# Kernel optimization log

Hardware: AMD Instinct MI355X
Metric: run time of the kernel (lower is better)

The kernel has to match this reference:

```python
import jax, jax.numpy as jnp
import numpy as np

N_EMBD = 1024
N_HEAD = 16
B, T, T_MEM = 4, 1024, 1024


def setup_inputs() -> dict:
    key = jax.random.key(0)
    ks = jax.random.split(key, 11)
    s = 1.0 / np.sqrt(N_EMBD)
    inp = {
        "q_in": jax.random.normal(ks[0], (B, T, N_EMBD), jnp.float32),
        "k_in": jax.random.normal(ks[1], (B, T_MEM, N_EMBD), jnp.float32),
        "v_in": jax.random.normal(ks[2], (B, T_MEM, N_EMBD), jnp.float32),
        "Wq": jax.random.normal(ks[3], (N_EMBD, N_EMBD), jnp.float32) * s,
        "bq": jnp.zeros((N_EMBD,), jnp.float32),
        "Wk": jax.random.normal(ks[4], (N_EMBD, N_EMBD), jnp.float32) * s,
        "bk": jnp.zeros((N_EMBD,), jnp.float32),
        "Wv": jax.random.normal(ks[5], (N_EMBD, N_EMBD), jnp.float32) * s,
        "bv": jnp.zeros((N_EMBD,), jnp.float32),
        "Wo": jax.random.normal(ks[6], (N_EMBD, N_EMBD), jnp.float32) * s,
        "bo": jnp.zeros((N_EMBD,), jnp.float32),
    }
    return inp


def reference(q_in, k_in, v_in, Wq, bq, Wk, bk, Wv, bv, Wo, bo):
    b, t, c = q_in.shape
    t_mem = k_in.shape[1]
    h = N_HEAD
    hs = c // h
    # torch Linear: x @ W.T + b
    q = (q_in @ Wq.T + bq).reshape(b, t, h, hs).transpose(0, 2, 1, 3)      # [b,h,t,hs]
    k = (k_in @ Wk.T + bk).reshape(b, t_mem, h, hs).transpose(0, 2, 1, 3)  # [b,h,tm,hs]
    v = (v_in @ Wv.T + bv).reshape(b, t_mem, h, hs).transpose(0, 2, 1, 3)
    att = jnp.einsum('bhtd,bhsd->bhts', q, k) * (1.0 / np.sqrt(hs))        # [b,h,t,tm]
    att = jax.nn.softmax(att, axis=-1)
    # dropout is identity (pdrop=0 / eval mode)
    y = jnp.einsum('bhts,bhsd->bhtd', att, v)                              # [b,h,t,hs]
    y = y.transpose(0, 2, 1, 3).reshape(b, t, c)
    y = y @ Wo.T + bo
    attention = att.mean(axis=1)                                           # [b,t,tm]
    return (y, attention)
```

## Files before the change

### kernel.cpp

```cpp
#include <hip/hip_runtime.h>

typedef unsigned short ushort_t;
typedef __attribute__((ext_vector_type(8))) __bf16 bf16x8;
typedef __attribute__((ext_vector_type(4))) float f32x4;

#define GLD(src, lds) __builtin_amdgcn_global_load_lds( \
    (const __attribute__((address_space(1))) void*)(src), \
    (__attribute__((address_space(3))) void*)(lds), 16, 0, 0)

#if __has_builtin(__builtin_amdgcn_exp2f)
#define EXP2(x) __builtin_amdgcn_exp2f(x)
#else
#define EXP2(x) __expf((x) * 0.69314718f)
#endif
#define QK_SCALE 0.18033688f

static __device__ __forceinline__ f32x4 mfma16(bf16x8 a, bf16x8 b, f32x4 c){
  return __builtin_amdgcn_mfma_f32_16x16x32_bf16(a, b, c, 0, 0, 0);
}
static __device__ __forceinline__ ushort_t f2bf(float f){
  unsigned u = __float_as_uint(f);
  return (ushort_t)((u + 0x7FFFu + ((u >> 16) & 1u)) >> 16);
}

template<int ROWS>
static __device__ __forceinline__ void stage64(const ushort_t* __restrict__ g, size_t rstride,
                                               ushort_t* lds, int tid){
#pragma unroll
  for (int r = 0; r < ROWS/32; ++r){
    int li = r*256 + tid;
    int row = li >> 3, ch = li & 7;
    GLD(g + (size_t)row*rstride + ((ch ^ (row & 7)) << 3),
        (char*)lds + (r*256 + (tid >> 6)*64)*16);
  }
}
static __device__ __forceinline__ bf16x8 frag64(const ushort_t* lds, int row, int ch){
  return *(const bf16x8*)((const char*)lds + row*128 + ((ch ^ (row & 7)) << 4));
}

static __device__ __forceinline__ void stage32(const ushort_t* __restrict__ g, size_t rstride,
                                               ushort_t* lds, int tid){
#pragma unroll
  for (int r = 0; r < 2; ++r){
    int li = r*256 + tid;
    int row = li >> 2, ch = li & 3;
    GLD(g + (size_t)row*rstride + ((ch ^ ((row >> 1) & 3)) << 3),
        (char*)lds + (r*256 + (tid >> 6)*64)*16);
  }
}
static __device__ __forceinline__ bf16x8 frag32(const ushort_t* lds, int row, int ch){
  return *(const bf16x8*)((const char*)lds + row*64 + ((ch ^ ((row >> 1) & 3)) << 4));
}

__global__ __launch_bounds__(256) void cast_all(const float* __restrict__ q,
    const float* __restrict__ k, const float* __restrict__ v,
    const float* __restrict__ wq, const float* __restrict__ wk,
    const float* __restrict__ wv, const float* __restrict__ wo,
    char* __restrict__ ws)
{
  const size_t MB = 1024*1024;
  int i = blockIdx.x*256 + threadIdx.x;
  const float* src; ushort_t* dst; int j;
  if (i < 1048576){ src = q; dst = (ushort_t*)(ws); j = i; }
  else if (i < 2097152){ src = k; dst = (ushort_t*)(ws + 8*MB); j = i - 1048576; }
  else if (i < 3145728){ src = v; dst = (ushort_t*)(ws + 16*MB); j = i - 2097152; }
  else {
    int t = i - 3145728, w = t >> 18; j = t & 262143;
    src = w==0 ? wq : w==1 ? wk : w==2 ? wv : wo;
    dst = (ushort_t*)(ws + (24 + 2*(size_t)w)*MB);
  }
  float4 x = ((const float4*)src)[j];
  ushort4 o;
  o.x = f2bf(x.x); o.y = f2bf(x.y); o.z = f2bf(x.z); o.w = f2bf(x.w);
  ((ushort4*)dst)[j] = o;
}

template<int MODE>
static __device__ __forceinline__ void gemm_body(const ushort_t* __restrict__ A,
    const ushort_t* __restrict__ B, const float* __restrict__ bias,
    void* __restrict__ Cout, int bx, char* smem)
{
  constexpr int K = 1024;
  ushort_t* As0 = (ushort_t*)smem;
  ushort_t* As1 = (ushort_t*)(smem + 8192);
  ushort_t* Bs0 = (ushort_t*)(smem + 16384);
  ushort_t* Bs1 = (ushort_t*)(smem + 24576);
  const int tid = threadIdx.x, lane = tid & 63, wv = tid >> 6;
  const int fr = lane & 15, fq = lane >> 4;
  const int wr = wv >> 1, wc = wv & 1;
  const int brow0 = ((bx & 7) * 4 + ((bx >> 3) & 3)) * 128;
  const int bcol0 = (bx >> 5) * 128;

  const f32x4 zero = {0.f, 0.f, 0.f, 0.f};
  f32x4 acc[4][4];
#pragma unroll
  for (int m = 0; m < 4; ++m)
#pragma unroll
    for (int n = 0; n < 4; ++n) acc[m][n] = zero;

  stage32(A + (size_t)brow0*K, K, As0, tid);
  stage32(B + (size_t)bcol0*K, K, Bs0, tid);
  __syncthreads();

  for (int kt = 0; kt < K/32; ++kt){
    const int cur = kt & 1;
    ushort_t* Ac = cur ? As1 : As0;
    ushort_t* Bc = cur ? Bs1 : Bs0;
    ushort_t* An = cur ? As0 : As1;
    ushort_t* Bn = cur ? Bs0 : Bs1;
    if (kt < K/32 - 1){
      stage32(A + (size_t)brow0*K + (kt+1)*32, K, An, tid);
      stage32(B + (size_t)bcol0*K + (kt+1)*32, K, Bn, tid);
    }
    bf16x8 af[4], bfg[4];
#pragma unroll
    for (int m = 0; m < 4; ++m) af[m]  = frag32(Ac, wr*64 + m*16 + fr, fq);
#pragma unroll
    for (int n = 0; n < 4; ++n) bfg[n] = frag32(Bc, wc*64 + n*16 + fr, fq);
    __builtin_amdgcn_s_setprio(1);
#pragma unroll
    for (int m = 0; m < 4; ++m)
#pragma unroll
      for (int n = 0; n < 4; ++n)
        acc[m][n] = mfma16(af[m], bfg[n], acc[m][n]);
    __builtin_amdgcn_s_setprio(0);
    __syncthreads();
  }

#pragma unroll
  for (int n = 0; n < 4; ++n){
    const int colg = bcol0 + wc*64 + n*16 + fr;
    const float bv = bias[colg];
#pragma unroll
    for (int m = 0; m < 4; ++m){
      const int rowg0 = brow0 + wr*64 + m*16 + fq*4;
      if (MODE == 1){
        int b = rowg0 >> 10, t = rowg0 & 1023, h = colg >> 6, d = colg & 63;
        ushort4 o;
        o.x = f2bf(acc[m][n][0] + bv); o.y = f2bf(acc[m][n][1] + bv);
        o.z = f2bf(acc[m][n][2] + bv); o.w = f2bf(acc[m][n][3] + bv);
        *(ushort4*)((ushort_t*)Cout + (((size_t)(b*16 + h))*64 + d)*1024 + t) = o;
      } else {
#pragma unroll
        for (int r = 0; r < 4; ++r){
          const int rowg = rowg0 + r;
          float val = acc[m][n][r] + bv;
          if (MODE == 0){
            int b = rowg >> 10, t = rowg & 1023, h = colg >> 6, d = colg & 63;
            ((ushort_t*)Cout)[(((size_t)(b*16 + h))*1024 + t)*64 + d] = f2bf(val);
          } else {
            ((float*)Cout)[(size_t)rowg*1024 + colg] = val;
          }
        }
      }
    }
  }
}

__global__ __launch_bounds__(256) void gemm_qkv(const ushort_t* qb, const ushort_t* kb,
    const ushort_t* vb, const ushort_t* wqb, const ushort_t* wkb, const ushort_t* wvb,
    const float* bq, const float* bk, const float* bv,
    ushort_t* Qm, ushort_t* Km, ushort_t* Vtm)
{
  __shared__ char smem[32768];
  int id = blockIdx.x >> 8, bx = blockIdx.x & 255;
  if (id == 0)      gemm_body<0>(qb, wqb, bq, Qm,  bx, smem);
  else if (id == 1) gemm_body<0>(kb, wkb, bk, Km,  bx, smem);
  else              gemm_body<1>(vb, wvb, bv, Vtm, bx, smem);
}

static __device__ __forceinline__ void attmean_body(const ushort_t* __restrict__ Q,
    const ushort_t* __restrict__ Kmat, const float* __restrict__ Lrow,
    float* __restrict__ attOut, int nb, char* smem)
{
  ushort_t* Qs0 = (ushort_t*)smem;
  ushort_t* Qs1 = (ushort_t*)(smem + 8192);
  ushort_t* Ks0 = (ushort_t*)(smem + 16384);
  ushort_t* Ks1 = (ushort_t*)(smem + 32768);
  const int tid = threadIdx.x, lane = tid & 63, wv = tid >> 6;
  const int fr = lane & 15, fq = lane >> 4;
  const int c_ = nb & 7, k_ = nb >> 3;
  const int b = c_ >> 1;
  const int rem = (c_ & 1)*64 + k_;
  const int t0 = (rem >> 3) * 64, s0 = (rem & 7) * 128;

  const f32x4 zero = {0.f, 0.f, 0.f, 0.f};
  f32x4 acc[2][4];
#pragma unroll
  for (int c = 0; c < 2; ++c)
#pragma unroll
    for (int n = 0; n < 4; ++n) acc[c][n] = zero;

  stage64<64>(Q + ((size_t)(b*16)*1024 + t0)*64, 64, Qs0, tid);
  stage64<128>(Kmat + ((size_t)(b*16)*1024 + s0)*64, 64, Ks0, tid);
  __syncthreads();

  for (int h = 0; h < 16; ++h){
    const int cur = h & 1;
    ushort_t* Qc = cur ? Qs1 : Qs0;
    ushort_t* Kc = cur ? Ks1 : Ks0;
    ushort_t* Qn = cur ? Qs0 : Qs1;
    ushort_t* Kn = cur ? Ks0 : Ks1;
    if (h < 15){
      stage64<64>(Q + ((size_t)(b*16 + h+1)*1024 + t0)*64, 64, Qn, tid);
      stage64<128>(Kmat + ((size_t)(b*16 + h+1)*1024 + s0)*64, 64, Kn, tid);
    }
    const int bh = b*16 + h;
    bf16x8 qf0 = frag64(Qc, wv*16 + fr, fq);
    bf16x8 qf1 = frag64(Qc, wv*16 + fr, 4 + fq);
    const float il = 1.f / Lrow[bh*1024 + t0 + wv*16 + fr];
#pragma unroll
    for (int c = 0; c < 2; ++c){
      f32x4 sfr[4];
      __builtin_amdgcn_s_setprio(1);
#pragma unroll
      for (int n = 0; n < 4; ++n){
        f32x4 s0v = mfma16(frag64(Kc, c*64 + n*16 + fr, fq), qf0, zero);
        sfr[n] = mfma16(frag64(Kc, c*64 + n*16 + fr, 4 + fq), qf1, s0v);
      }
      __builtin_amdgcn_s_setprio(0);
#pragma unroll
      for (int n = 0; n < 4; ++n)
#pragma unroll
        for (int r = 0; r < 4; ++r)
          acc[c][n][r] += EXP2(sfr[n][r] * QK_SCALE) * il;
    }
    __syncthreads();
  }

  const float s16 = 1.f/16.f;
#pragma unroll
  for (int c = 0; c < 2; ++c)
#pragma unroll
    for (int n = 0; n < 4; ++n){
      f32x4 v = acc[c][n];
      v[0] *= s16; v[1] *= s16; v[2] *= s16; v[3] *= s16;
      size_t idx = ((size_t)b << 20) + (size_t)(t0 + wv*16 + fr)*1024 + s0 + c*64 + n*16 + fq*4;
      *(f32x4*)(attOut + idx) = v;
    }
}

__global__ __launch_bounds__(256) void fused_tail(const ushort_t* __restrict__ Yws,
    const ushort_t* __restrict__ Wob, const float* __restrict__ bo, float* __restrict__ y_out,
    const ushort_t* __restrict__ Qm, const ushort_t* __restrict__ Km,
    const float* __restrict__ Lrow, float* __restrict__ att_out)
{
  __shared__ char smem[49152];
  const int bx = blockIdx.x;
  if (bx < 256) gemm_body<2>(Yws, Wob, bo, y_out, bx, smem);
  else          attmean_body(Qm, Km, Lrow, att_out, bx - 256, smem);
}

__global__ __launch_bounds__(256, 2) void flash_kernel(const ushort_t* __restrict__ Q,
                                                       const ushort_t* __restrict__ Kmat,
                                                       const ushort_t* __restrict__ Vt,
                                                       ushort_t* __restrict__ Yws,
                                                       float* __restrict__ Lrow)
{
  __shared__ ushort_t Ks[2][64][64];
  __shared__ ushort_t Vts[2][64][64];
  __shared__ ushort_t Ps[4][32][64];
  const int tid = threadIdx.x, lane = tid & 63, wv = tid >> 6;
  const int fr = lane & 15, fq = lane >> 4;
  const int nb = blockIdx.x;
  const int bh = (nb & 7)*8 + (nb >> 6);
  const int t0 = ((nb >> 3) & 7) * 128;

  stage64<128>(Q + ((size_t)bh*1024 + t0)*64, 64, &Ps[0][0][0], tid);
  stage64<64>(Kmat + (size_t)bh*1024*64, 64, &Ks[0][0][0], tid);
  stage64<64>(Vt + (size_t)bh*64*1024, 1024, &Vts[0][0][0], tid);
  __syncthreads();
  bf16x8 aQ[2][2];
#pragma unroll
  for (int mt = 0; mt < 2; ++mt)
#pragma unroll
    for (int h = 0; h < 2; ++h)
      aQ[mt][h] = frag64(&Ps[0][0][0], wv*32 + mt*16 + fr, h*4 + fq);
  __syncthreads();

  bf16x8 ones;
#pragma unroll
  for (int i = 0; i < 8; ++i) ones[i] = (__bf16)1.0f;

  const f32x4 zero = {0.f, 0.f, 0.f, 0.f};
  f32x4 o_acc[2][4], l_acc[2];
#pragma unroll
  for (int mt = 0; mt < 2; ++mt){
    l_acc[mt] = zero;
#pragma unroll
    for (int n = 0; n < 4; ++n) o_acc[mt][n] = zero;
  }
  char* myP = (char*)&Ps[wv][0][0];

  for (int sc = 0; sc < 16; ++sc){
    const int cur = sc & 1;
    if (sc < 15){
      stage64<64>(Kmat + ((size_t)bh*1024 + (sc+1)*64)*64, 64, &Ks[cur^1][0][0], tid);
      stage64<64>(Vt + (size_t)bh*64*1024 + (sc+1)*64, 1024, &Vts[cur^1][0][0], tid);
    }
    bf16x8 kf[4][2];
#pragma unroll
    for (int n = 0; n < 4; ++n){
      kf[n][0] = frag64(&Ks[cur][0][0], n*16 + fr, fq);
      kf[n][1] = frag64(&Ks[cur][0][0], n*16 + fr, 4 + fq);
    }
    f32x4 sfr[2][4];
    __builtin_amdgcn_s_setprio(1);
#pragma unroll
    for (int mt = 0; mt < 2; ++mt)
#pragma unroll
      for (int n = 0; n < 4; ++n){
        f32x4 s0 = mfma16(kf[n][0], aQ[mt][0], zero);
        sfr[mt][n] = mfma16(kf[n][1], aQ[mt][1], s0);
      }
    __builtin_amdgcn_s_setprio(0);
#pragma unroll
    for (int mt = 0; mt < 2; ++mt){
#pragma unroll
      for (int n = 0; n < 4; ++n){
        float p0 = EXP2(sfr[mt][n][0] * QK_SCALE);
        float p1 = EXP2(sfr[mt][n][1] * QK_SCALE);
        float p2 = EXP2(sfr[mt][n][2] * QK_SCALE);
        float p3 = EXP2(sfr[mt][n][3] * QK_SCALE);
        uint2 w;
        w.x = (unsigned)f2bf(p0) | ((unsigned)f2bf(p1) << 16);
        w.y = (unsigned)f2bf(p2) | ((unsigned)f2bf(p3) << 16);
        *(uint2*)(myP + mt*2048 + fr*128 + (((n*4 + fq) ^ (fr & 14)) << 3)) = w;
      }
    }
    asm volatile("s_waitcnt lgkmcnt(0)" ::: "memory");
    __builtin_amdgcn_sched_barrier(0);
    __builtin_amdgcn_s_setprio(1);
#pragma unroll
    for (int ks = 0; ks < 2; ++ks){
      bf16x8 pa[2];
#pragma unroll
      for (int mt = 0; mt < 2; ++mt){
        uint4 u = *(const uint4*)(myP + mt*2048 + fr*128 + (((ks*8 + fq*2) ^ (fr & 14)) << 3));
        pa[mt] = __builtin_bit_cast(bf16x8, u);
      }
#pragma unroll
      for (int n = 0; n < 4; ++n){
        bf16x8 vf = frag64(&Vts[cur][0][0], n*16 + fr, ks*4 + fq);
#pragma unroll
        for (int mt = 0; mt < 2; ++mt)
          o_acc[mt][n] = mfma16(pa[mt], vf, o_acc[mt][n]);
      }
#pragma unroll
      for (int mt = 0; mt < 2; ++mt)
        l_acc[mt] = mfma16(pa[mt], ones, l_acc[mt]);
    }
    __builtin_amdgcn_s_setprio(0);
    __syncthreads();
  }

  const int b = bh >> 4, h = bh & 15;
#pragma unroll
  for (int mt = 0; mt < 2; ++mt){
    float inv[4];
#pragma unroll
    for (int r = 0; r < 4; ++r) inv[r] = 1.f / l_acc[mt][r];
#pragma unroll
    for (int n = 0; n < 4; ++n)
#pragma unroll
      for (int r = 0; r < 4; ++r){
        size_t row = (size_t)b*1024 + t0 + wv*32 + mt*16 + fq*4 + r;
        Yws[row*1024 + h*64 + n*16 + fr] = f2bf(o_acc[mt][n][r] * inv[r]);
      }
  }
  if (fr == 0){
#pragma unroll
    for (int mt = 0; mt < 2; ++mt)
#pragma unroll
      for (int r = 0; r < 4; ++r)
        Lrow[bh*1024 + t0 + wv*32 + mt*16 + fq*4 + r] = l_acc[mt][r];
  }
}

extern "C" void kernel_launch(void* const* d_in, const int* in_sizes, int n_in,
                              void* d_out, int out_size, void* d_ws, size_t ws_size,
                              hipStream_t stream)
{
  const float* q_in = (const float*)d_in[0];
  const float* k_in = (const float*)d_in[1];
  const float* v_in = (const float*)d_in[2];
  const float* Wq   = (const float*)d_in[3];
  const float* bq   = (const float*)d_in[4];
  const float* Wk   = (const float*)d_in[5];
  const float* bk   = (const float*)d_in[6];
  const float* Wv   = (const float*)d_in[7];
  const float* bv   = (const float*)d_in[8];
  const float* Wo   = (const float*)d_in[9];
  const float* bo   = (const float*)d_in[10];

  float* y_out   = (float*)d_out;
  float* att_out = y_out + (size_t)4*1024*1024;

  char* ws = (char*)d_ws;
  const size_t MB = 1024*1024;
  ushort_t* qb   = (ushort_t*)(ws + 0);
  ushort_t* kb   = (ushort_t*)(ws + 8*MB);
  ushort_t* vb   = (ushort_t*)(ws + 16*MB);
  ushort_t* wqb  = (ushort_t*)(ws + 24*MB);
  ushort_t* wkb  = (ushort_t*)(ws + 26*MB);
  ushort_t* wvb  = (ushort_t*)(ws + 28*MB);
  ushort_t* wob  = (ushort_t*)(ws + 30*MB);
  ushort_t* Qm   = (ushort_t*)(ws + 32*MB);
  ushort_t* Km   = (ushort_t*)(ws + 40*MB);
  ushort_t* Vtm  = (ushort_t*)(ws + 48*MB);
  ushort_t* Yws  = (ushort_t*)(ws + 56*MB);
  float*    Lrow = (float*)(ws + 64*MB);

  cast_all<<<16384, 256, 0, stream>>>(q_in, k_in, v_in, Wq, Wk, Wv, Wo, ws);

  gemm_qkv<<<768, 256, 0, stream>>>(qb, kb, vb, wqb, wkb, wvb, bq, bk, bv, Qm, Km, Vtm);

  flash_kernel<<<512, 256, 0, stream>>>(Qm, Km, Vtm, Yws, Lrow);

  fused_tail<<<768, 256, 0, stream>>>(Yws, wob, bo, y_out, Qm, Km, Lrow, att_out);
}
```

Measured before the change: 131.4 us.

## Triple-buffer GEMM K-tiles with counted vmcnt waits and single barrier

Replaces the double-buffered GEMM main loop with a three-stage LDS ring that prefetches two K-tiles ahead. It uses explicit s_waitcnt vmcnt(4) plus a raw s_barrier instead of __syncthreads, so async global-to-LDS loads can stay in flight across iterations. It also turns the templated MODE into a runtime argument so one code path serves all projection GEMMs. The cost is more shared memory (48KB), which may lower occupancy, and runtime mode branches in the epilogue.

```diff
diff --git a/kernel.cpp b/kernel.cpp
--- a/kernel.cpp
+++ b/kernel.cpp
@@ -75,16 +75,11 @@
   ((ushort4*)dst)[j] = o;
 }
 
-template<int MODE>
 static __device__ __forceinline__ void gemm_body(const ushort_t* __restrict__ A,
     const ushort_t* __restrict__ B, const float* __restrict__ bias,
-    void* __restrict__ Cout, int bx, char* smem)
+    void* __restrict__ Cout, int bx, int mode, char* smem)
 {
   constexpr int K = 1024;
-  ushort_t* As0 = (ushort_t*)smem;
-  ushort_t* As1 = (ushort_t*)(smem + 8192);
-  ushort_t* Bs0 = (ushort_t*)(smem + 16384);
-  ushort_t* Bs1 = (ushort_t*)(smem + 24576);
   const int tid = threadIdx.x, lane = tid & 63, wv = tid >> 6;
   const int fr = lane & 15, fq = lane >> 4;
   const int wr = wv >> 1, wc = wv & 1;
@@ -98,20 +93,24 @@
 #pragma unroll
     for (int n = 0; n < 4; ++n) acc[m][n] = zero;
 
-  stage32(A + (size_t)brow0*K, K, As0, tid);
-  stage32(B + (size_t)bcol0*K, K, Bs0, tid);
-  __syncthreads();
-
-  for (int kt = 0; kt < K/32; ++kt){
-    const int cur = kt & 1;
-    ushort_t* Ac = cur ? As1 : As0;
-    ushort_t* Bc = cur ? Bs1 : Bs0;
-    ushort_t* An = cur ? As0 : As1;
-    ushort_t* Bn = cur ? Bs0 : Bs1;
-    if (kt < K/32 - 1){
-      stage32(A + (size_t)brow0*K + (kt+1)*32, K, An, tid);
-      stage32(B + (size_t)bcol0*K + (kt+1)*32, K, Bn, tid);
-    }
+  const ushort_t* Abase = A + (size_t)brow0*K;
+  const ushort_t* Bbase = B + (size_t)bcol0*K;
+
+  stage32(Abase,      K, (ushort_t*)(smem),             tid);
+  stage32(Bbase,      K, (ushort_t*)(smem + 24576),     tid);
+  stage32(Abase + 32, K, (ushort_t*)(smem + 8192),      tid);
+  stage32(Bbase + 32, K, (ushort_t*)(smem + 24576 + 8192), tid);
+  asm volatile("s_waitcnt vmcnt(4)" ::: "memory");
+  __builtin_amdgcn_s_barrier();
+
+  int rd = 0, wrb = 2;
+  for (int kt = 0; kt < 32; ++kt){
+    if (kt < 30){
+      stage32(Abase + (kt+2)*32, K, (ushort_t*)(smem + wrb*8192),         tid);
+      stage32(Bbase + (kt+2)*32, K, (ushort_t*)(smem + 24576 + wrb*8192), tid);
+    }
+    const ushort_t* Ac = (const ushort_t*)(smem + rd*8192);
+    const ushort_t* Bc = (const ushort_t*)(smem + 24576 + rd*8192);
     bf16x8 af[4], bfg[4];
 #pragma unroll
     for (int m = 0; m < 4; ++m) af[m]  = frag32(Ac, wr*64 + m*16 + fr, fq);
@@ -124,7 +123,12 @@
       for (int n = 0; n < 4; ++n)
         acc[m][n] = mfma16(af[m], bfg[n], acc[m][n]);
     __builtin_amdgcn_s_setprio(0);
-    __syncthreads();
+    __builtin_amdgcn_sched_barrier(0);
+    if (kt < 30) asm volatile("s_waitcnt vmcnt(4)" ::: "memory");
+    else         asm volatile("s_waitcnt vmcnt(0)" ::: "memory");
+    __builtin_amdgcn_s_barrier();
+    rd  = (rd  == 2) ? 0 : rd  + 1;
+    wrb = (wrb == 2) ? 0 : wrb + 1;
   }
 
 #pragma unroll
@@ -134,7 +138,7 @@
 #pragma unroll
     for (int m = 0; m < 4; ++m){
       const int rowg0 = brow0 + wr*64 + m*16 + fq*4;
-      if (MODE == 1){
+      if (mode == 1){
         int b = rowg0 >> 10, t = rowg0 & 1023, h = colg >> 6, d = colg & 63;
         ushort4 o;
         o.x = f2bf(acc[m][n][0] + bv); o.y = f2bf(acc[m][n][1] + bv);
@@ -145,7 +149,7 @@
         for (int r = 0; r < 4; ++r){
           const int rowg = rowg0 + r;
           float val = acc[m][n][r] + bv;
-          if (MODE == 0){
+          if (mode == 0){
             int b = rowg >> 10, t = rowg & 1023, h = colg >> 6, d = colg & 63;
             ((ushort_t*)Cout)[(((size_t)(b*16 + h))*1024 + t)*64 + d] = f2bf(val);
           } else {
@@ -162,11 +166,13 @@
     const float* bq, const float* bk, const float* bv,
     ushort_t* Qm, ushort_t* Km, ushort_t* Vtm)
 {
-  __shared__ char smem[32768];
+  __shared__ char smem[49152];
   int id = blockIdx.x >> 8, bx = blockIdx.x & 255;
-  if (id == 0)      gemm_body<0>(qb, wqb, bq, Qm,  bx, smem);
-  else if (id == 1) gemm_body<0>(kb, wkb, bk, Km,  bx, smem);
-  else              gemm_body<1>(vb, wvb, bv, Vtm, bx, smem);
+  const ushort_t* A = id==0 ? qb : id==1 ? kb : vb;
+  const ushort_t* B = id==0 ? wqb : id==1 ? wkb : wvb;
+  const float* bias = id==0 ? bq : id==1 ? bk : bv;
+  void* C = id==0 ? (void*)Qm : id==1 ? (void*)Km : (void*)Vtm;
+  gemm_body(A, B, bias, C, bx, id==2 ? 1 : 0, smem);
 }
 
 static __device__ __forceinline__ void attmean_body(const ushort_t* __restrict__ Q,
@@ -247,7 +253,7 @@
 {
   __shared__ char smem[49152];
   const int bx = blockIdx.x;
-  if (bx < 256) gemm_body<2>(Yws, Wob, bo, y_out, bx, smem);
+  if (bx < 256) gemm_body(Yws, Wob, bo, y_out, bx, 2, smem);
   else          attmean_body(Qm, Km, Lrow, att_out, bx - 256, smem);
 }
 
```

Result: faster. 128.2 us (-2.5%).
